# Optimization experiments

Measured on AMD Instinct MI355X. Metric: run time of the kernel, lower is better.

Reference implementation:

```python
import jax, jax.numpy as jnp
import numpy as np

B, S, E, H = 2, 2048, 1024, 16
D = E // H  # head_dim = 64


def setup_inputs() -> dict:
    key = jax.random.key(0)
    ks = jax.random.split(key, 4)
    return {
        "hidden_states": jax.random.normal(ks[0], (B, S, E), jnp.float32),
        "qk_weight": jax.random.normal(ks[1], (E, 2 * E), jnp.float32) * 0.02,
        "qk_bias": jnp.zeros((2 * E,), jnp.float32),
        "v_weight": jax.random.normal(ks[2], (E, E), jnp.float32) * 0.02,
        "v_resid_gain": jnp.ones((), jnp.float32),
        "v_skip_gain": jnp.ones((), jnp.float32),
        "proj_weight": jax.random.normal(ks[3], (E, E), jnp.float32) * 0.02,
        "proj_resid_gain": jnp.ones((), jnp.float32),
        "proj_skip_gain": jnp.ones((), jnp.float32),
        "attn_mat_resid_gain": jnp.ones((H,), jnp.float32),
        "attn_mat_skip_gain": jnp.ones((H,), jnp.float32),
        "centre_attn_gain": jnp.ones((H,), jnp.float32),
    }


def reference(hidden_states, qk_weight, qk_bias, v_weight, v_resid_gain,
              v_skip_gain, proj_weight, proj_resid_gain, proj_skip_gain,
              attn_mat_resid_gain, attn_mat_skip_gain, centre_attn_gain):
    b, s, e = hidden_states.shape
    dt = hidden_states.dtype
    eye_e = jnp.eye(e, dtype=dt)

    # qk_attn: MyConv1D (standard linear), split into query/key
    qk = hidden_states @ qk_weight + qk_bias
    q, k = jnp.split(qk, 2, axis=-1)
    # v_attn: skip MyConv1D -> x @ (resid_gain * W + skip_gain * I), no bias
    v = hidden_states @ (v_resid_gain * v_weight + v_skip_gain * eye_e)

    def split_heads(t):  # [b,s,e] -> [b,h,s,d]
        return t.reshape(b, s, H, D).transpose(0, 2, 1, 3)

    q, k, v = split_heads(q), split_heads(k), split_heads(v)

    # scaled causal attention scores
    scores = jnp.einsum('bhqd,bhkd->bhqk', q, k) / jnp.asarray(D, dt) ** 0.5
    causal = jnp.tril(jnp.ones((s, s), bool))
    scores = jnp.where(causal, scores, jnp.finfo(dt).min)
    attn = jax.nn.softmax(scores, axis=-1)

    # shaped attention: gain-mix softmax probs with identity and causal-uniform
    uniform = jnp.tril(jnp.ones((s, s), dt) / jnp.arange(1, s + 1, dtype=dt)[:, None])
    g_r = attn_mat_resid_gain[None, :, None, None]
    g_s = attn_mat_skip_gain[None, :, None, None]
    g_c = centre_attn_gain[None, :, None, None]
    new_attn = g_r * attn + g_s * jnp.eye(s, dtype=dt) - g_c * uniform

    ctx = jnp.einsum('bhqk,bhkd->bhqd', new_attn, v)
    ctx = ctx.transpose(0, 2, 1, 3).reshape(b, s, e)  # merge heads
    # c_proj: skip MyConv1D, no bias
    out = ctx @ (proj_resid_gain * proj_weight + proj_skip_gain * eye_e)
    return out
```

## Files before the change

### kernel.cpp

```cpp
#include <hip/hip_runtime.h>

typedef __bf16 bf16;
typedef __attribute__((ext_vector_type(8))) __bf16 bf16x8;
typedef __attribute__((ext_vector_type(4))) float f32x4;

union U16x8 { uint4 u; bf16 h[8]; };
union Pack4 { uint2 u2; bf16 h[4]; };

#define QSCALE 0.18033688011112042f

__device__ __forceinline__ void async16(const bf16* g, bf16* l) {
    __builtin_amdgcn_global_load_lds((const __attribute__((address_space(1))) void*)g,
                                     (__attribute__((address_space(3))) void*)l, 16, 0, 0);
}
__device__ __forceinline__ void async4(const bf16* g, bf16* l) {
    __builtin_amdgcn_global_load_lds((const __attribute__((address_space(1))) void*)g,
                                     (__attribute__((address_space(3))) void*)l, 4, 0, 0);
}

__device__ const int QT_OF[40] = {15,15,15,15,14,14,14,14,13,13,13,13,12,12,12,12,
                                  11,11,11,10,10,10,9,9,9,8,8,8,7,7,6,6,5,5,4,4,3,2,1,0};
__device__ const int CK_OF[40] = {0,1,2,3,0,1,2,3,0,1,2,3,0,1,2,3,
                                  0,1,2,0,1,2,0,1,2,0,1,2,0,1,0,1,0,1,0,1,0,0,0,0};
__device__ const int BASE_OF[16] = {39,38,37,36,34,32,30,28,25,22,19,16,12,8,4,0};

__global__ void prep(const float* __restrict__ hs, bf16* __restrict__ hsb,
                     const float* __restrict__ qkw, const float* __restrict__ vw,
                     const float* __restrict__ pw, bf16* __restrict__ qkvT,
                     bf16* __restrict__ pwT, float* __restrict__ csum,
                     const float* __restrict__ vrg, const float* __restrict__ vsg,
                     const float* __restrict__ prg, const float* __restrict__ psg) {
    const int K = 1024;
    int bx = blockIdx.x;
    if (bx < 8) {
        float4* p = (float4*)csum + (bx * 256 + threadIdx.x) * 16;
        #pragma unroll
        for (int i = 0; i < 16; i++) p[i] = make_float4(0.f, 0.f, 0.f, 0.f);
        return;
    }
    if (bx < 4104) {
        int i = ((bx - 8) * 256 + threadIdx.x) * 4;
        float4 f = *(const float4*)(hs + i);
        hsb[i + 0] = (bf16)f.x; hsb[i + 1] = (bf16)f.y;
        hsb[i + 2] = (bf16)f.z; hsb[i + 3] = (bf16)f.w;
        return;
    }
    int r = bx - 4104;
    int z = r < 2048 ? 0 : (r < 3072 ? 1 : 2);
    int q = z == 0 ? r : (z == 1 ? r - 2048 : r - 3072);
    int ntiles = z == 0 ? 64 : 32;
    int N = z == 0 ? 2048 : 1024;
    const float* W = z == 0 ? qkw : (z == 1 ? vw : pw);
    bf16* WT = z == 0 ? qkvT : (z == 1 ? qkvT + (size_t)2 * 1024 * 1024 : pwT);
    float g0 = z == 0 ? 1.f : (z == 1 ? vrg[0] : prg[0]);
    float g1 = z == 0 ? 0.f : (z == 1 ? vsg[0] : psg[0]);

    __shared__ float tile[32][33];
    int n0 = (q % ntiles) * 32, k0 = (q / ntiles) * 32;
    int tx = threadIdx.x & 31, ty = threadIdx.x >> 5;
    #pragma unroll
    for (int rr = 0; rr < 32; rr += 8)
        tile[ty + rr][tx] = W[(size_t)(k0 + ty + rr) * N + n0 + tx];
    __syncthreads();
    #pragma unroll
    for (int rr = 0; rr < 32; rr += 8) {
        int n = n0 + ty + rr, k = k0 + tx;
        float v = g0 * tile[tx][ty + rr] + ((n == k) ? g1 : 0.f);
        if (z == 0 && n < 1024) v *= QSCALE;
        WT[(size_t)n * K + k] = (bf16)v;
    }
}

template<int BN>
__global__ __launch_bounds__(256, 3)
void gemm_bt(const bf16* __restrict__ A, const bf16* __restrict__ BT,
             int M, int N, int K, void* __restrict__ Cout,
             bf16* __restrict__ C2T, float* __restrict__ csum,
             int mode, const float* __restrict__ aux) {
    __shared__ __align__(16) bf16 As[128][64];
    __shared__ __align__(16) bf16 Bs[BN][64];
    constexpr int JF = BN / 32;
    int bid = blockIdx.x;
    int g32 = bid & 31;
    int m0 = ((g32 & 7) * 4 + (g32 >> 3)) * 128;
    int n0 = (bid >> 5) * BN;
    int t = threadIdx.x, lane = t & 63, w = t >> 6;
    int wm = (w >> 1) * 64, wn = (w & 1) * (BN / 2);
    int lrow = lane & 15, lkg = lane >> 4;

    f32x4 acc[4][JF] = {};

    int gsw = ((lane & 7) ^ ((lane >> 3) & 7)) * 8;
    const bf16* Ab = A + (size_t)(m0 + w * 8 + (lane >> 3)) * K + gsw;
    const bf16* Bb = BT + (size_t)(n0 + w * 8 + (lane >> 3)) * K + gsw;

    for (int k0 = 0; k0 < K; k0 += 64) {
        #pragma unroll
        for (int p = 0; p < 4; p++)
            async16(Ab + (size_t)(p * 32) * K + k0, &As[p * 32 + w * 8][0]);
        #pragma unroll
        for (int p = 0; p < BN / 32; p++)
            async16(Bb + (size_t)(p * 32) * K + k0, &Bs[p * 32 + w * 8][0]);
        __syncthreads();
        #pragma unroll
        for (int ks = 0; ks < 2; ks++) {
            bf16x8 af[4], bfr[JF];
            int phys = (((4 * ks + lkg) ^ (lrow & 7)) << 3);
            #pragma unroll
            for (int i = 0; i < 4; i++) af[i] = *(const bf16x8*)&As[wm + i * 16 + lrow][phys];
            #pragma unroll
            for (int j = 0; j < JF; j++) bfr[j] = *(const bf16x8*)&Bs[wn + j * 16 + lrow][phys];
            #pragma unroll
            for (int i = 0; i < 4; i++)
                #pragma unroll
                for (int j = 0; j < JF; j++)
                    acc[i][j] = __builtin_amdgcn_mfma_f32_16x16x32_bf16(af[i], bfr[j], acc[i][j], 0, 0, 0);
        }
        __syncthreads();
    }

    int rgrp = (lane >> 4) * 4;
    #pragma unroll
    for (int i = 0; i < 4; i++) {
        #pragma unroll
        for (int j = 0; j < JF; j++) {
            int col = n0 + wn + j * 16 + lrow;
            int row0 = m0 + wm + i * 16 + rgrp;
            if (mode == 0) {
                if (col < 2048) {
                    float bb = aux[col];
                    if (col < 1024) bb *= QSCALE;
                    #pragma unroll
                    for (int reg = 0; reg < 4; reg++)
                        ((bf16*)Cout)[(size_t)(row0 + reg) * 2048 + col] = (bf16)(acc[i][j][reg] + bb);
                } else {
                    int c = col - 2048;
                    Pack4 p4;
                    #pragma unroll
                    for (int reg = 0; reg < 4; reg++) p4.h[reg] = (bf16)acc[i][j][reg];
                    *(uint2*)&C2T[(size_t)c * 4096 + row0] = p4.u2;
                }
            } else {
                #pragma unroll
                for (int reg = 0; reg < 4; reg++)
                    ((float*)Cout)[(size_t)(row0 + reg) * N + col] = acc[i][j][reg];
            }
        }
    }

    if (mode == 0 && n0 >= 2048) {
        int chunkb = (m0 + wm) >> 5;
        #pragma unroll
        for (int j = 0; j < JF; j++) {
            float s0 = 0.f, s1 = 0.f;
            #pragma unroll
            for (int reg = 0; reg < 4; reg++) {
                s0 += acc[0][j][reg] + acc[1][j][reg];
                s1 += acc[2][j][reg] + acc[3][j][reg];
            }
            s0 += __shfl_xor(s0, 16, 64); s0 += __shfl_xor(s0, 32, 64);
            s1 += __shfl_xor(s1, 16, 64); s1 += __shfl_xor(s1, 32, 64);
            if (lkg == 0) {
                int col = n0 - 2048 + wn + j * 16 + lrow;
                atomicAdd(&csum[(size_t)col * 128 + chunkb], s0);
                atomicAdd(&csum[(size_t)col * 128 + chunkb + 1], s1);
            }
        }
    }
}

__global__ __launch_bounds__(256, 3)
void flash_split(const bf16* __restrict__ qk, const bf16* __restrict__ vT,
                 bf16* __restrict__ Opart, float* __restrict__ lbuf,
                 int S, int E, int H) {
    __shared__ __align__(16) bf16 smem[25600];
    #define KS(bu, r, c) smem[(bu) * 4096 + (r) * 64 + (c)]
    #define VT(bu, r, c) smem[8192 + (bu) * 4096 + (r) * 64 + (c)]

    int item = blockIdx.x, bh = blockIdx.y;
    int qt = QT_OF[item], ck = CK_OF[item];
    int b = bh >> 4, h = bh & 15;
    int q0 = qt * 128;
    int ktstart = ck * 8;
    int nloc = min(8, 2 * (qt + 1) - ktstart);
    int t = threadIdx.x, lane = t & 63, w = t >> 6;
    int lrow = lane & 15, lkg = lane >> 4;
    const int ld = 2 * E;

    const bf16* Qg  = qk + (size_t)(b * S + q0) * ld + h * 64;
    const bf16* Kg0 = qk + (size_t)(b * S) * ld + E + h * 64;
    const bf16* Vg0 = vT + (size_t)(h * 64) * 4096 + b * 2048;

    bf16x8 qf[2][2];
    #pragma unroll
    for (int qg = 0; qg < 2; qg++)
        #pragma unroll
        for (int ks = 0; ks < 2; ks++)
            qf[qg][ks] = *(const bf16x8*)&Qg[(size_t)(32 * w + 16 * qg + lrow) * ld + ks * 32 + lkg * 8];

    f32x4 oacc[4][2] = {};
    float lrun[2] = {0.f, 0.f};

    auto stage = [&](int buf, int kt) {
        int k0 = kt * 64;
        int gg = (lane & 7) ^ ((lane >> 3) & 7);
        #pragma unroll
        for (int p = 0; p < 2; p++) {
            int row = w * 8 + p * 32 + (lane >> 3);
            async16(Kg0 + (size_t)(k0 + row) * ld + gg * 8, &KS(buf, row, (lane & 7) * 8));
        }
        int gcol = lane & 31;
        #pragma unroll
        for (int it = 0; it < 8; it++) {
            int row = it * 8 + w * 2 + (lane >> 5);
            int lb = (gcol >> 2) ^ (row & 7);
            int kk = ((lb >> 2) << 5) | (((gcol >> 1) & 1) << 4)
                   | ((lb & 3) << 2) | ((gcol & 1) << 1);
            async4(Vg0 + (size_t)row * 4096 + k0 + kk, &VT(buf, row, gcol * 2));
        }
    };

    stage(0, ktstart);
    for (int kl = 0; kl < nloc; kl++) {
        int buf = kl & 1;
        int k0 = (ktstart + kl) * 64;
        __syncthreads();
        if (kl + 1 < nloc) stage(1 - buf, ktstart + kl + 1);

        bool skip0 = (k0 > q0 + 32 * w + 15);
        bool skip1 = (k0 > q0 + 32 * w + 31);
        if (skip0 && skip1) continue;

        f32x4 sacc[2][4] = {};
        #pragma unroll
        for (int ks = 0; ks < 2; ks++) {
            bf16x8 ak[4];
            int phys = (((4 * ks + lkg) ^ (lrow & 7)) << 3);
            #pragma unroll
            for (int kf = 0; kf < 4; kf++)
                ak[kf] = *(const bf16x8*)&KS(buf, 16 * kf + lrow, phys);
            #pragma unroll
            for (int kf = 0; kf < 4; kf++)
                sacc[0][kf] = __builtin_amdgcn_mfma_f32_16x16x32_bf16(ak[kf], qf[0][ks], sacc[0][kf], 0, 0, 0);
            if (!skip1)
                #pragma unroll
                for (int kf = 0; kf < 4; kf++)
                    sacc[1][kf] = __builtin_amdgcn_mfma_f32_16x16x32_bf16(ak[kf], qf[1][ks], sacc[1][kf], 0, 0, 0);
        }

        bf16x8 bp[2][2];
        #pragma unroll
        for (int qg = 0; qg < 2; qg++) {
            if ((qg == 0 && skip0) || (qg == 1 && skip1)) continue;
            int kmin = q0 + 32 * w + 16 * qg;
            float rsum = 0.f;
            if (k0 + 63 <= kmin) {
                #pragma unroll
                for (int kf = 0; kf < 4; kf++)
                    #pragma unroll
                    for (int r = 0; r < 4; r++) {
                        float p = exp2f(sacc[qg][kf][r]);
                        rsum += p;
                        bp[qg][kf >> 1][(kf & 1) * 4 + r] = (bf16)p;
                    }
            } else {
                int qrow = kmin + lrow;
                #pragma unroll
                for (int kf = 0; kf < 4; kf++)
                    #pragma unroll
                    for (int r = 0; r < 4; r++) {
                        float sv = sacc[qg][kf][r];
                        if (k0 + 16 * kf + 4 * lkg + r > qrow) sv = -1e30f;
                        float p = exp2f(sv);
                        rsum += p;
                        bp[qg][kf >> 1][(kf & 1) * 4 + r] = (bf16)p;
                    }
            }
            lrun[qg] += rsum;
        }

        #pragma unroll
        for (int ks = 0; ks < 2; ks++) {
            bf16x8 av[4];
            int phys = (((4 * ks + lkg) ^ (lrow & 7)) << 3);
            #pragma unroll
            for (int df = 0; df < 4; df++)
                av[df] = *(const bf16x8*)&VT(buf, 16 * df + lrow, phys);
            #pragma unroll
            for (int qg = 0; qg < 2; qg++) {
                if ((qg == 0 && skip0) || (qg == 1 && skip1)) continue;
                #pragma unroll
                for (int df = 0; df < 4; df++)
                    oacc[df][qg] = __builtin_amdgcn_mfma_f32_16x16x32_bf16(av[df], bp[qg][ks], oacc[df][qg], 0, 0, 0);
            }
        }
    }

    __syncthreads();
    bf16* eps = smem;
    size_t ibase = (size_t)(bh * 40 + item) * 128;
    #pragma unroll
    for (int qg = 0; qg < 2; qg++) {
        #pragma unroll
        for (int df = 0; df < 4; df++) {
            Pack4 p4;
            #pragma unroll
            for (int r = 0; r < 4; r++) p4.h[r] = (bf16)oacc[df][qg][r];
            *(uint2*)&eps[(size_t)(w * 32 + 16 * qg + lrow) * 72 + 16 * df + 4 * lkg] = p4.u2;
        }
        float l = lrun[qg];
        l += __shfl_xor(l, 16, 64);
        l += __shfl_xor(l, 32, 64);
        if (lkg == 0) lbuf[ibase + w * 32 + qg * 16 + lrow] = l;
    }
    int r_l = lane >> 1, half = lane & 1;
    bf16* orow = Opart + (ibase + w * 32 + r_l) * 64 + 32 * half;
    #pragma unroll
    for (int c = 0; c < 4; c++)
        *(uint4*)&orow[8 * c] = *(const uint4*)&eps[(size_t)(w * 32 + r_l) * 72 + 32 * half + 8 * c];
    #undef KS
    #undef VT
}

__global__ void merge_combine(const bf16* __restrict__ Opart, const float* __restrict__ lbuf,
                              const bf16* __restrict__ vT, const float* __restrict__ csum,
                              const float* __restrict__ gr, const float* __restrict__ gs,
                              const float* __restrict__ gc, bf16* __restrict__ ctx) {
    const int S = 2048, E = 1024;
    int qt = blockIdx.x, bh = blockIdx.y;
    int b = bh >> 4, h = bh & 15;
    int nc = (qt >> 2) + 1, base = BASE_OF[qt];
    int q0 = qt * 128;
    int t = threadIdx.x;

    __shared__ bf16 osm[128][66];

    {
        int r = t >> 1, dh = (t & 1) * 32;
        float L = 0.f;
        for (int c = 0; c < nc; c++)
            L += lbuf[(size_t)(bh * 40 + base + c) * 128 + r];
        float inv = 1.f / L;
        float o[32] = {};
        for (int c = 0; c < nc; c++) {
            const bf16* src = Opart + ((size_t)(bh * 40 + base + c) * 128 + r) * 64 + dh;
            #pragma unroll
            for (int g = 0; g < 4; g++) {
                U16x8 u; u.u = *(const uint4*)&src[g * 8];
                #pragma unroll
                for (int j = 0; j < 8; j++) o[g * 8 + j] += (float)u.h[j];
            }
        }
        #pragma unroll
        for (int j = 0; j < 32; j++) osm[r][dh + j] = (bf16)(o[j] * inv);
    }
    __syncthreads();

    {
        int c = t & 63, sc = t >> 6;
        int col = h * 64 + c;
        int row0 = q0 + sc * 32;
        float grh = gr[h], gsh = gs[h], gch = gc[h];
        int cend = qt * 4 + sc;
        const float4* cs4 = (const float4*)(csum + (size_t)col * 128 + b * 64);
        float run = 0.f;
        #pragma unroll
        for (int g = 0; g < 16; g++) {
            float4 f = cs4[g];
            int j = g * 4;
            run += (j + 0 < cend ? f.x : 0.f) + (j + 1 < cend ? f.y : 0.f)
                 + (j + 2 < cend ? f.z : 0.f) + (j + 3 < cend ? f.w : 0.f);
        }
        const bf16* vrow = vT + (size_t)col * 4096 + b * 2048 + row0;
        U16x8 vv[4];
        #pragma unroll
        for (int g = 0; g < 4; g++) vv[g].u = *(const uint4*)&vrow[g * 8];
        bf16* cp = ctx + ((size_t)(b * S + row0)) * E + col;
        #pragma unroll
        for (int i = 0; i < 32; i++) {
            float v = (float)vv[i >> 3].h[i & 7];
            run += v;
            float pm = run / (float)(row0 + i + 1);
            cp[(size_t)i * E] = (bf16)(grh * (float)osm[sc * 32 + i][c] + gsh * v - gch * pm);
        }
    }
}

extern "C" void kernel_launch(void* const* d_in, const int* in_sizes, int n_in,
                              void* d_out, int out_size, void* d_ws, size_t ws_size,
                              hipStream_t stream) {
    const float* hs  = (const float*)d_in[0];
    const float* qkw = (const float*)d_in[1];
    const float* qkb = (const float*)d_in[2];
    const float* vw  = (const float*)d_in[3];
    const float* vrg = (const float*)d_in[4];
    const float* vsg = (const float*)d_in[5];
    const float* pw  = (const float*)d_in[6];
    const float* prg = (const float*)d_in[7];
    const float* psg = (const float*)d_in[8];
    const float* amr = (const float*)d_in[9];
    const float* ams = (const float*)d_in[10];
    const float* amc = (const float*)d_in[11];
    float* out = (float*)d_out;

    const int B = 2, S = 2048, E = 1024, H = 16, M = B * S;
    char* ws = (char*)d_ws;
    size_t off = 0;
    auto alloc = [&](size_t bytes) { void* p = ws + off; off += (bytes + 255) & ~255ull; return p; };
    bf16* hsb   = (bf16*)alloc((size_t)M * E * 2);
    bf16* qkvT  = (bf16*)alloc((size_t)3 * E * E * 2);
    bf16* pwT   = (bf16*)alloc((size_t)E * E * 2);
    bf16* qko   = (bf16*)alloc((size_t)M * 2 * E * 2);
    bf16* vT    = (bf16*)alloc((size_t)E * M * 2);
    float* csum = (float*)alloc((size_t)E * 128 * 4);
    bf16* ctxb  = (bf16*)alloc((size_t)M * E * 2);
    bf16* Opart = (bf16*)alloc((size_t)32 * 40 * 128 * 64 * 2);
    float* lbuf = (float*)alloc((size_t)32 * 40 * 128 * 4);

    prep<<<8200, 256, 0, stream>>>(hs, hsb, qkw, vw, pw, qkvT, pwT, csum, vrg, vsg, prg, psg);

    gemm_bt<128><<<32 * (3 * E / 128), 256, 0, stream>>>(
        hsb, qkvT, M, 3 * E, E, qko, vT, csum, 0, qkb);

    flash_split<<<dim3(40, 32), 256, 0, stream>>>(qko, vT, Opart, lbuf, S, E, H);
    merge_combine<<<dim3(16, 32), 256, 0, stream>>>(Opart, lbuf, vT, csum, amr, ams, amc, ctxb);

    gemm_bt<64><<<32 * (E / 64), 256, 0, stream>>>(
        ctxb, pwT, M, E, E, out, nullptr, nullptr, 2, nullptr);
}
```

Baseline: 205.0 us.

## Pair adjacent query tiles in one 512-thread block to share K/V staging

Each flash block now processes two adjacent query tiles (one per 4-wave half) over the same key chunk, so each K/V tile is staged into LDS once and used by twice as many waves. The grid halves and block size doubles, the LDS array shrinks, and the epilogue is serialised per half with extra barriers. The row-sum accumulation is also rewritten as a tree. The cost is some imbalance when the two tiles have different causal extents (the lower tile idles on the last tiles) and more barrier participants.

```diff
diff --git a/kernel.cpp b/kernel.cpp
--- a/kernel.cpp
+++ b/kernel.cpp
@@ -18,11 +18,13 @@
                                      (__attribute__((address_space(3))) void*)l, 4, 0, 0);
 }
 
-__device__ const int QT_OF[40] = {15,15,15,15,14,14,14,14,13,13,13,13,12,12,12,12,
-                                  11,11,11,10,10,10,9,9,9,8,8,8,7,7,6,6,5,5,4,4,3,2,1,0};
-__device__ const int CK_OF[40] = {0,1,2,3,0,1,2,3,0,1,2,3,0,1,2,3,
-                                  0,1,2,0,1,2,0,1,2,0,1,2,0,1,0,1,0,1,0,1,0,0,0,0};
 __device__ const int BASE_OF[16] = {39,38,37,36,34,32,30,28,25,22,19,16,12,8,4,0};
+
+__device__ const int P_QTA[20] = {15,15,15,15,13,13,13,13,11,11,11,9,9,9,7,7,5,5,3,1};
+__device__ const int P_QTB[20] = {14,14,14,14,12,12,12,12,10,10,10,8,8,8,6,6,4,4,2,0};
+__device__ const int P_CK [20] = { 0, 1, 2, 3, 0, 1, 2, 3, 0, 1, 2,0,1,2,0,1,0,1,0,0};
+__device__ const int P_IA [20] = { 0, 1, 2, 3, 8, 9,10,11,16,17,18,22,23,24,28,29,32,33,36,38};
+__device__ const int P_IB [20] = { 4, 5, 6, 7,12,13,14,15,19,20,21,25,26,27,30,31,34,35,37,39};
 
 __global__ void prep(const float* __restrict__ hs, bf16* __restrict__ hsb,
                      const float* __restrict__ qkw, const float* __restrict__ vw,
@@ -169,25 +171,27 @@
     }
 }
 
-__global__ __launch_bounds__(256, 3)
+__global__ __launch_bounds__(512, 4)
 void flash_split(const bf16* __restrict__ qk, const bf16* __restrict__ vT,
                  bf16* __restrict__ Opart, float* __restrict__ lbuf,
                  int S, int E, int H) {
-    __shared__ __align__(16) bf16 smem[25600];
+    __shared__ __align__(16) bf16 smem[16384];
     #define KS(bu, r, c) smem[(bu) * 4096 + (r) * 64 + (c)]
     #define VT(bu, r, c) smem[8192 + (bu) * 4096 + (r) * 64 + (c)]
 
-    int item = blockIdx.x, bh = blockIdx.y;
-    int qt = QT_OF[item], ck = CK_OF[item];
+    int pair = blockIdx.x, bh = blockIdx.y;
+    int qtA = P_QTA[pair], qtB = P_QTB[pair], ck = P_CK[pair];
     int b = bh >> 4, h = bh & 15;
-    int q0 = qt * 128;
     int ktstart = ck * 8;
-    int nloc = min(8, 2 * (qt + 1) - ktstart);
+    int nloc = min(8, 2 * (qtA + 1) - ktstart);
     int t = threadIdx.x, lane = t & 63, w = t >> 6;
+    int wl = w & 3, hf = w >> 2;
+    int qth = hf ? qtB : qtA;
+    int q0h = qth * 128;
     int lrow = lane & 15, lkg = lane >> 4;
     const int ld = 2 * E;
 
-    const bf16* Qg  = qk + (size_t)(b * S + q0) * ld + h * 64;
+    const bf16* Qg  = qk + (size_t)(b * S + q0h) * ld + h * 64;
     const bf16* Kg0 = qk + (size_t)(b * S) * ld + E + h * 64;
     const bf16* Vg0 = vT + (size_t)(h * 64) * 4096 + b * 2048;
 
@@ -196,7 +200,7 @@
     for (int qg = 0; qg < 2; qg++)
         #pragma unroll
         for (int ks = 0; ks < 2; ks++)
-            qf[qg][ks] = *(const bf16x8*)&Qg[(size_t)(32 * w + 16 * qg + lrow) * ld + ks * 32 + lkg * 8];
+            qf[qg][ks] = *(const bf16x8*)&Qg[(size_t)(32 * wl + 16 * qg + lrow) * ld + ks * 32 + lkg * 8];
 
     f32x4 oacc[4][2] = {};
     float lrun[2] = {0.f, 0.f};
@@ -204,15 +208,14 @@
     auto stage = [&](int buf, int kt) {
         int k0 = kt * 64;
         int gg = (lane & 7) ^ ((lane >> 3) & 7);
-        #pragma unroll
-        for (int p = 0; p < 2; p++) {
-            int row = w * 8 + p * 32 + (lane >> 3);
+        {
+            int row = w * 8 + (lane >> 3);
             async16(Kg0 + (size_t)(k0 + row) * ld + gg * 8, &KS(buf, row, (lane & 7) * 8));
         }
         int gcol = lane & 31;
         #pragma unroll
-        for (int it = 0; it < 8; it++) {
-            int row = it * 8 + w * 2 + (lane >> 5);
+        for (int it = 0; it < 4; it++) {
+            int row = it * 16 + w * 2 + (lane >> 5);
             int lb = (gcol >> 2) ^ (row & 7);
             int kk = ((lb >> 2) << 5) | (((gcol >> 1) & 1) << 4)
                    | ((lb & 3) << 2) | ((gcol & 1) << 1);
@@ -227,8 +230,8 @@
         __syncthreads();
         if (kl + 1 < nloc) stage(1 - buf, ktstart + kl + 1);
 
-        bool skip0 = (k0 > q0 + 32 * w + 15);
-        bool skip1 = (k0 > q0 + 32 * w + 31);
+        bool skip0 = (k0 > q0h + 32 * wl + 15);
+        bool skip1 = (k0 > q0h + 32 * wl + 31);
         if (skip0 && skip1) continue;
 
         f32x4 sacc[2][4] = {};
@@ -252,31 +255,35 @@
         #pragma unroll
         for (int qg = 0; qg < 2; qg++) {
             if ((qg == 0 && skip0) || (qg == 1 && skip1)) continue;
-            int kmin = q0 + 32 * w + 16 * qg;
-            float rsum = 0.f;
+            int kmin = q0h + 32 * wl + 16 * qg;
+            float rs[4];
             if (k0 + 63 <= kmin) {
                 #pragma unroll
-                for (int kf = 0; kf < 4; kf++)
+                for (int kf = 0; kf < 4; kf++) {
+                    float p[4];
                     #pragma unroll
                     for (int r = 0; r < 4; r++) {
-                        float p = exp2f(sacc[qg][kf][r]);
-                        rsum += p;
-                        bp[qg][kf >> 1][(kf & 1) * 4 + r] = (bf16)p;
+                        p[r] = exp2f(sacc[qg][kf][r]);
+                        bp[qg][kf >> 1][(kf & 1) * 4 + r] = (bf16)p[r];
                     }
+                    rs[kf] = (p[0] + p[1]) + (p[2] + p[3]);
+                }
             } else {
                 int qrow = kmin + lrow;
                 #pragma unroll
-                for (int kf = 0; kf < 4; kf++)
+                for (int kf = 0; kf < 4; kf++) {
+                    float p[4];
                     #pragma unroll
                     for (int r = 0; r < 4; r++) {
                         float sv = sacc[qg][kf][r];
                         if (k0 + 16 * kf + 4 * lkg + r > qrow) sv = -1e30f;
-                        float p = exp2f(sv);
-                        rsum += p;
-                        bp[qg][kf >> 1][(kf & 1) * 4 + r] = (bf16)p;
+                        p[r] = exp2f(sv);
+                        bp[qg][kf >> 1][(kf & 1) * 4 + r] = (bf16)p[r];
                     }
-            }
-            lrun[qg] += rsum;
+                    rs[kf] = (p[0] + p[1]) + (p[2] + p[3]);
+                }
+            }
+            lrun[qg] += (rs[0] + rs[1]) + (rs[2] + rs[3]);
         }
 
         #pragma unroll
@@ -297,27 +304,36 @@
     }
 
     __syncthreads();
-    bf16* eps = smem;
-    size_t ibase = (size_t)(bh * 40 + item) * 128;
-    #pragma unroll
-    for (int qg = 0; qg < 2; qg++) {
-        #pragma unroll
-        for (int df = 0; df < 4; df++) {
-            Pack4 p4;
-            #pragma unroll
-            for (int r = 0; r < 4; r++) p4.h[r] = (bf16)oacc[df][qg][r];
-            *(uint2*)&eps[(size_t)(w * 32 + 16 * qg + lrow) * 72 + 16 * df + 4 * lkg] = p4.u2;
-        }
-        float l = lrun[qg];
-        l += __shfl_xor(l, 16, 64);
-        l += __shfl_xor(l, 32, 64);
-        if (lkg == 0) lbuf[ibase + w * 32 + qg * 16 + lrow] = l;
-    }
-    int r_l = lane >> 1, half = lane & 1;
-    bf16* orow = Opart + (ibase + w * 32 + r_l) * 64 + 32 * half;
-    #pragma unroll
-    for (int c = 0; c < 4; c++)
-        *(uint4*)&orow[8 * c] = *(const uint4*)&eps[(size_t)(w * 32 + r_l) * 72 + 32 * half + 8 * c];
+    {
+        bf16* eps = smem;
+        int itemh = hf ? P_IB[pair] : P_IA[pair];
+        size_t ibase = (size_t)(bh * 40 + itemh) * 128;
+        #pragma unroll
+        for (int ph = 0; ph < 2; ph++) {
+            if (hf == ph) {
+                #pragma unroll
+                for (int qg = 0; qg < 2; qg++) {
+                    #pragma unroll
+                    for (int df = 0; df < 4; df++) {
+                        Pack4 p4;
+                        #pragma unroll
+                        for (int r = 0; r < 4; r++) p4.h[r] = (bf16)oacc[df][qg][r];
+                        *(uint2*)&eps[(size_t)(wl * 32 + 16 * qg + lrow) * 72 + 16 * df + 4 * lkg] = p4.u2;
+                    }
+                    float l = lrun[qg];
+                    l += __shfl_xor(l, 16, 64);
+                    l += __shfl_xor(l, 32, 64);
+                    if (lkg == 0) lbuf[ibase + wl * 32 + qg * 16 + lrow] = l;
+                }
+                int r_l = lane >> 1, half2 = lane & 1;
+                bf16* orow = Opart + (ibase + wl * 32 + r_l) * 64 + 32 * half2;
+                #pragma unroll
+                for (int c = 0; c < 4; c++)
+                    *(uint4*)&orow[8 * c] = *(const uint4*)&eps[(size_t)(wl * 32 + r_l) * 72 + 32 * half2 + 8 * c];
+            }
+            __syncthreads();
+        }
+    }
     #undef KS
     #undef VT
 }
@@ -422,7 +438,7 @@
     gemm_bt<128><<<32 * (3 * E / 128), 256, 0, stream>>>(
         hsb, qkvT, M, 3 * E, E, qko, vT, csum, 0, qkb);
 
-    flash_split<<<dim3(40, 32), 256, 0, stream>>>(qko, vT, Opart, lbuf, S, E, H);
+    flash_split<<<dim3(20, 32), 512, 0, stream>>>(qko, vT, Opart, lbuf, S, E, H);
     merge_combine<<<dim3(16, 32), 256, 0, stream>>>(Opart, lbuf, vT, csum, amr, ams, amc, ctxb);
 
     gemm_bt<64><<<32 * (E / 64), 256, 0, stream>>>(
```

New measurement: 251.1 us. 1.22x slower.

## Triple-buffer K/V tiles in flash_split with vmcnt-based waits

Applied to the files above, without the earlier changes.

Moves the flash attention split kernel from double to triple buffering of K and V^T tiles in LDS. Prefetch now runs two tiles ahead, and each iteration uses an explicit s_waitcnt vmcnt plus a raw barrier in place of __syncthreads, so loads for later tiles can stay in flight. The row-sum reduction is also reordered into a tree to shorten the dependent add chain. The risks are that the hardcoded vmcnt count must match the number of async loads issued per stage, and the per-block LDS footprint changes, which could affect occupancy.

```diff
diff --git a/kernel.cpp b/kernel.cpp
--- a/kernel.cpp
+++ b/kernel.cpp
@@ -173,9 +173,9 @@
 void flash_split(const bf16* __restrict__ qk, const bf16* __restrict__ vT,
                  bf16* __restrict__ Opart, float* __restrict__ lbuf,
                  int S, int E, int H) {
-    __shared__ __align__(16) bf16 smem[25600];
-    #define KS(bu, r, c) smem[(bu) * 4096 + (r) * 64 + (c)]
-    #define VT(bu, r, c) smem[8192 + (bu) * 4096 + (r) * 64 + (c)]
+    __shared__ __align__(16) bf16 smem[24576];
+    #define KS(bu, r, c) smem[(bu) * 8192 + (r) * 64 + (c)]
+    #define VT(bu, r, c) smem[(bu) * 8192 + 4096 + (r) * 64 + (c)]
 
     int item = blockIdx.x, bh = blockIdx.y;
     int qt = QT_OF[item], ck = CK_OF[item];
@@ -221,11 +221,21 @@
     };
 
     stage(0, ktstart);
+    stage(1, ktstart + 1);
+
     for (int kl = 0; kl < nloc; kl++) {
-        int buf = kl & 1;
+        int buf = kl % 3;
         int k0 = (ktstart + kl) * 64;
-        __syncthreads();
-        if (kl + 1 < nloc) stage(1 - buf, ktstart + kl + 1);
+
+        if (kl + 1 < nloc) {
+            asm volatile("s_waitcnt vmcnt(10)" ::: "memory");
+        } else {
+            asm volatile("s_waitcnt vmcnt(0)" ::: "memory");
+        }
+        __builtin_amdgcn_s_barrier();
+        __builtin_amdgcn_sched_barrier(0);
+
+        if (kl + 2 < nloc) stage((kl + 2) % 3, ktstart + kl + 2);
 
         bool skip0 = (k0 > q0 + 32 * w + 15);
         bool skip1 = (k0 > q0 + 32 * w + 31);
@@ -253,30 +263,34 @@
         for (int qg = 0; qg < 2; qg++) {
             if ((qg == 0 && skip0) || (qg == 1 && skip1)) continue;
             int kmin = q0 + 32 * w + 16 * qg;
-            float rsum = 0.f;
+            float rs[4];
             if (k0 + 63 <= kmin) {
                 #pragma unroll
-                for (int kf = 0; kf < 4; kf++)
+                for (int kf = 0; kf < 4; kf++) {
+                    float p[4];
                     #pragma unroll
                     for (int r = 0; r < 4; r++) {
-                        float p = exp2f(sacc[qg][kf][r]);
-                        rsum += p;
-                        bp[qg][kf >> 1][(kf & 1) * 4 + r] = (bf16)p;
+                        p[r] = exp2f(sacc[qg][kf][r]);
+                        bp[qg][kf >> 1][(kf & 1) * 4 + r] = (bf16)p[r];
                     }
+                    rs[kf] = (p[0] + p[1]) + (p[2] + p[3]);
+                }
             } else {
                 int qrow = kmin + lrow;
                 #pragma unroll
-                for (int kf = 0; kf < 4; kf++)
+                for (int kf = 0; kf < 4; kf++) {
+                    float p[4];
                     #pragma unroll
                     for (int r = 0; r < 4; r++) {
                         float sv = sacc[qg][kf][r];
                         if (k0 + 16 * kf + 4 * lkg + r > qrow) sv = -1e30f;
-                        float p = exp2f(sv);
-                        rsum += p;
-                        bp[qg][kf >> 1][(kf & 1) * 4 + r] = (bf16)p;
+                        p[r] = exp2f(sv);
+                        bp[qg][kf >> 1][(kf & 1) * 4 + r] = (bf16)p[r];
                     }
-            }
-            lrun[qg] += rsum;
+                    rs[kf] = (p[0] + p[1]) + (p[2] + p[3]);
+                }
+            }
+            lrun[qg] += (rs[0] + rs[1]) + (rs[2] + rs[3]);
         }
 
         #pragma unroll
```

Result: no change. 208.7 us (+1.8%).

## Reorder flash work items heavy-first and compute row sums via MFMA

Applied to the files above, without the earlier changes.

Flattens the flash grid to 1D and dispatches full 8-tile work items for all heads before the lighter, shorter items, aiming to reduce tail imbalance. The softmax row sums are now accumulated by an MFMA against a ones vector instead of scalar adds plus cross-lane shuffles, and the bf16-rounded probabilities are summed, which slightly changes numerics. The code also uses the hardware exp2 and reciprocal intrinsics in place of exp2f and division, at some cost in precision.

```diff
diff --git a/kernel.cpp b/kernel.cpp
--- a/kernel.cpp
+++ b/kernel.cpp
@@ -23,6 +23,9 @@
 __device__ const int CK_OF[40] = {0,1,2,3,0,1,2,3,0,1,2,3,0,1,2,3,
                                   0,1,2,0,1,2,0,1,2,0,1,2,0,1,0,1,0,1,0,1,0,0,0,0};
 __device__ const int BASE_OF[16] = {39,38,37,36,34,32,30,28,25,22,19,16,12,8,4,0};
+
+__device__ const int HV_IT[28] = {0,1,2,3,4,5,6,8,9,10,12,13,14,16,17,18,19,20,22,23,25,26,28,29,30,32,34,36};
+__device__ const int LT_IT[12] = {7,21,31,37,11,24,33,38,15,27,35,39};
 
 __global__ void prep(const float* __restrict__ hs, bf16* __restrict__ hsb,
                      const float* __restrict__ qkw, const float* __restrict__ vw,
@@ -177,7 +180,11 @@
     #define KS(bu, r, c) smem[(bu) * 4096 + (r) * 64 + (c)]
     #define VT(bu, r, c) smem[8192 + (bu) * 4096 + (r) * 64 + (c)]
 
-    int item = blockIdx.x, bh = blockIdx.y;
+    int g = blockIdx.x;
+    int item, bh;
+    if (g < 896) { bh = g / 28; item = HV_IT[g % 28]; }
+    else { int g2 = g - 896; bh = g2 / 12; item = LT_IT[g2 % 12]; }
+
     int qt = QT_OF[item], ck = CK_OF[item];
     int b = bh >> 4, h = bh & 15;
     int q0 = qt * 128;
@@ -198,8 +205,11 @@
         for (int ks = 0; ks < 2; ks++)
             qf[qg][ks] = *(const bf16x8*)&Qg[(size_t)(32 * w + 16 * qg + lrow) * ld + ks * 32 + lkg * 8];
 
+    const bf16 one = (bf16)1.0f;
+    const bf16x8 vones = {one, one, one, one, one, one, one, one};
+
     f32x4 oacc[4][2] = {};
-    float lrun[2] = {0.f, 0.f};
+    f32x4 lacc[2] = {};
 
     auto stage = [&](int buf, int kt) {
         int k0 = kt * 64;
@@ -253,16 +263,13 @@
         for (int qg = 0; qg < 2; qg++) {
             if ((qg == 0 && skip0) || (qg == 1 && skip1)) continue;
             int kmin = q0 + 32 * w + 16 * qg;
-            float rsum = 0.f;
             if (k0 + 63 <= kmin) {
                 #pragma unroll
                 for (int kf = 0; kf < 4; kf++)
                     #pragma unroll
-                    for (int r = 0; r < 4; r++) {
-                        float p = exp2f(sacc[qg][kf][r]);
-                        rsum += p;
-                        bp[qg][kf >> 1][(kf & 1) * 4 + r] = (bf16)p;
-                    }
+                    for (int r = 0; r < 4; r++)
+                        bp[qg][kf >> 1][(kf & 1) * 4 + r] =
+                            (bf16)__builtin_amdgcn_exp2f(sacc[qg][kf][r]);
             } else {
                 int qrow = kmin + lrow;
                 #pragma unroll
@@ -271,12 +278,11 @@
                     for (int r = 0; r < 4; r++) {
                         float sv = sacc[qg][kf][r];
                         if (k0 + 16 * kf + 4 * lkg + r > qrow) sv = -1e30f;
-                        float p = exp2f(sv);
-                        rsum += p;
-                        bp[qg][kf >> 1][(kf & 1) * 4 + r] = (bf16)p;
+                        bp[qg][kf >> 1][(kf & 1) * 4 + r] = (bf16)__builtin_amdgcn_exp2f(sv);
                     }
             }
-            lrun[qg] += rsum;
+            lacc[qg] = __builtin_amdgcn_mfma_f32_16x16x32_bf16(vones, bp[qg][0], lacc[qg], 0, 0, 0);
+            lacc[qg] = __builtin_amdgcn_mfma_f32_16x16x32_bf16(vones, bp[qg][1], lacc[qg], 0, 0, 0);
         }
 
         #pragma unroll
@@ -308,10 +314,7 @@
             for (int r = 0; r < 4; r++) p4.h[r] = (bf16)oacc[df][qg][r];
             *(uint2*)&eps[(size_t)(w * 32 + 16 * qg + lrow) * 72 + 16 * df + 4 * lkg] = p4.u2;
         }
-        float l = lrun[qg];
-        l += __shfl_xor(l, 16, 64);
-        l += __shfl_xor(l, 32, 64);
-        if (lkg == 0) lbuf[ibase + w * 32 + qg * 16 + lrow] = l;
+        if (lkg == 0) lbuf[ibase + w * 32 + qg * 16 + lrow] = lacc[qg][0];
     }
     int r_l = lane >> 1, half = lane & 1;
     bf16* orow = Opart + (ibase + w * 32 + r_l) * 64 + 32 * half;
@@ -380,7 +383,7 @@
         for (int i = 0; i < 32; i++) {
             float v = (float)vv[i >> 3].h[i & 7];
             run += v;
-            float pm = run / (float)(row0 + i + 1);
+            float pm = run * __builtin_amdgcn_rcpf((float)(row0 + i + 1));
             cp[(size_t)i * E] = (bf16)(grh * (float)osm[sc * 32 + i][c] + gsh * v - gch * pm);
         }
     }
@@ -422,7 +425,7 @@
     gemm_bt<128><<<32 * (3 * E / 128), 256, 0, stream>>>(
         hsb, qkvT, M, 3 * E, E, qko, vT, csum, 0, qkb);
 
-    flash_split<<<dim3(40, 32), 256, 0, stream>>>(qko, vT, Opart, lbuf, S, E, H);
+    flash_split<<<1280, 256, 0, stream>>>(qko, vT, Opart, lbuf, S, E, H);
     merge_combine<<<dim3(16, 32), 256, 0, stream>>>(Opart, lbuf, vT, csum, amr, ams, amc, ctxb);
 
     gemm_bt<64><<<32 * (E / 64), 256, 0, stream>>>(
```

Result: faster. 194.3 us (median of 2 runs) (-5.2%).
